# Kernel tuning notes

Hardware: AMD Instinct MI355X
Metric: run time of the kernel (lower is better)

The kernel has to match this reference:

```python
import jax, jax.numpy as jnp
import numpy as np

B, S, UNI, H, FLD = 64, 512, 1024, 1024, 256


def setup_inputs() -> dict:
    key = jax.random.key(0)
    ks = jax.random.split(key, 8)
    input_embeddings = jax.random.normal(ks[0], (B, S, UNI), dtype=jnp.float32)
    field_embeddings = jax.random.normal(ks[1], (B, S, FLD), dtype=jnp.float32)
    input_length = jax.random.randint(ks[2], (B,), 1, S + 1).astype(jnp.int32)
    # Force max length == S so the torch while-loop would run exactly S steps.
    input_length = input_length.at[0].set(S)
    std = 0.02
    W = jax.random.normal(ks[3], (UNI + H, 4 * H), dtype=jnp.float32) * std   # input+hidden -> i,j,f,o
    bW = jnp.zeros((4 * H,), dtype=jnp.float32)
    W1 = jax.random.normal(ks[4], (FLD, 2 * H), dtype=jnp.float32) * std      # field -> r,d
    bW1 = jnp.zeros((2 * H,), dtype=jnp.float32)
    return {
        "input_embeddings": input_embeddings,
        "field_embeddings": field_embeddings,
        "input_length": input_length,
        "W": W, "bW": bW, "W1": W1, "bW1": bW1,
    }


def reference(input_embeddings, field_embeddings, input_length, W, bW, W1, bW1):
    Bb, T, _ = input_embeddings.shape
    Hh = bW.shape[0] // 4
    # Field gate contribution is state-independent: precompute for all timesteps.
    fg = jnp.einsum('btf,fo->bto', field_embeddings, W1) + bW1      # [B,T,2H]
    r, d = jnp.split(fg, 2, axis=-1)
    field_term = jax.nn.sigmoid(r) * jnp.tanh(d)                    # [B,T,H]

    xs = jnp.swapaxes(input_embeddings, 0, 1)                       # [T,B,UNI]
    fts = jnp.swapaxes(field_term, 0, 1)                            # [T,B,H]
    # active[t,b] = t < input_length[b]  (mirrors `finished = t >= input_length`)
    active = jnp.arange(T, dtype=input_length.dtype)[:, None] < input_length[None, :]  # [T,B]

    h0 = jnp.zeros((Bb, Hh), dtype=input_embeddings.dtype)
    c0 = jnp.zeros((Bb, Hh), dtype=input_embeddings.dtype)

    def step(carry, inp):
        h, c = carry
        x_t, ft_t, act_t = inp
        gates = jnp.concatenate([x_t, h], axis=-1) @ W + bW         # [B,4H]
        i, j, f, o = jnp.split(gates, 4, axis=-1)
        c_new = jax.nn.sigmoid(f + 1.0) * c + jax.nn.sigmoid(i) * jnp.tanh(j) + ft_t
        h_new = jax.nn.sigmoid(o) * jnp.tanh(c_new)
        m = act_t[:, None]
        out = jnp.where(m, h_new, 0.0)                              # finished rows emit zeros
        h = jnp.where(m, h_new, h)                                  # finished rows keep prev state
        c = jnp.where(m, c_new, c)
        return (h, c), out

    (h_fin, c_fin), outs = jax.lax.scan(step, (h0, c0), (xs, fts, active))
    emit = jnp.swapaxes(outs, 0, 1)                                 # [B,T,H]
    return emit, (h_fin, c_fin)
```

## Files before the change

### kernel.cpp

```cpp
#include <hip/hip_runtime.h>

typedef unsigned short u16;
typedef __attribute__((ext_vector_type(8))) __bf16 bf16x8;
typedef __attribute__((ext_vector_type(4))) float f32x4;
typedef __attribute__((ext_vector_type(4))) unsigned int u32x4;
typedef __attribute__((ext_vector_type(2))) unsigned int u32x2;

#define GX_OFF   0ull
#define FT_OFF   268435456ull
#define WT_OFF   335544320ull
#define W1T_OFF  352321536ull
#define CB_OFF   352321536ull
#define HF_OFF   352583680ull
#define HB_OFF   353370112ull
#define WS_NEED  (HB_OFF + 262144ull)

#define NBLK 256

__device__ __forceinline__ float b2f(u16 u) {
    unsigned x = ((unsigned)u) << 16;
    return __builtin_bit_cast(float, x);
}
__device__ __forceinline__ u16 f2b(float f) {
    unsigned u = __builtin_bit_cast(unsigned, f);
    unsigned r = (u + 0x7FFFu + ((u >> 16) & 1u)) >> 16;
    return (u16)r;
}
__device__ __forceinline__ float fsigm(float x) {
    return __builtin_amdgcn_rcpf(1.f + __expf(-x));
}
__device__ __forceinline__ float ftanh2(float x) {
    return 2.f * __builtin_amdgcn_rcpf(1.f + __expf(-2.f * x)) - 1.f;
}
__device__ __forceinline__ bf16x8 ld_frag(const u16* p) {
    u32x4 v = *(const u32x4*)p;
    return __builtin_bit_cast(bf16x8, v);
}
__device__ __forceinline__ f32x4 mfma16(bf16x8 a, bf16x8 b, f32x4 c) {
    return __builtin_amdgcn_mfma_f32_16x16x32_bf16(a, b, c, 0, 0, 0);
}
__device__ __forceinline__ u32x4 cvt8(const float* p) {
    f32x4 a = *(const f32x4*)p;
    f32x4 b = *(const f32x4*)(p + 4);
    u32x4 r;
    r.x = (unsigned)f2b(a[0]) | ((unsigned)f2b(a[1]) << 16);
    r.y = (unsigned)f2b(a[2]) | ((unsigned)f2b(a[3]) << 16);
    r.z = (unsigned)f2b(b[0]) | ((unsigned)f2b(b[1]) << 16);
    r.w = (unsigned)f2b(b[2]) | ((unsigned)f2b(b[3]) << 16);
    return r;
}

__device__ __forceinline__ u32x4 ld16_coh(const u16* p) {
    u32x4 v;
    asm volatile("global_load_dwordx4 %0, %1, off sc0 sc1" : "=v"(v) : "v"(p));
    return v;
}
__device__ __forceinline__ void st2_coh(u16* p, u16 val) {
    unsigned v = val;
    asm volatile("global_store_short %0, %1, off sc0 sc1" :: "v"(p), "v"(v) : "memory");
}
__device__ __forceinline__ void st4_coh(unsigned* p, unsigned v) {
    asm volatile("global_store_dword %0, %1, off sc0 sc1" :: "v"(p), "v"(v) : "memory");
}
__device__ __forceinline__ unsigned ld4_coh_wait(const unsigned* p) {
    unsigned v;
    asm volatile("global_load_dword %0, %1, off sc0 sc1\n\ts_waitcnt vmcnt(0)"
                 : "=v"(v) : "v"(p) : "memory");
    return v;
}

__global__ void k_transpose(const float* __restrict__ in, u16* __restrict__ out, int R, int C) {
    __shared__ u16 tl[64][65];
    int tx = threadIdx.x, ty = threadIdx.y;
    int c0 = blockIdx.x * 64, r0 = blockIdx.y * 64;
#pragma unroll
    for (int i = 0; i < 16; i++) {
        int a = ty + i * 4;
        tl[a][tx] = f2b(in[(size_t)(r0 + a) * C + c0 + tx]);
    }
    __syncthreads();
#pragma unroll
    for (int i = 0; i < 16; i++) {
        int a = ty + i * 4;
        out[(size_t)(c0 + a) * R + r0 + tx] = tl[tx][a];
    }
}

__global__ __launch_bounds__(256) void k_field(const float* __restrict__ F, const u16* __restrict__ W1t,
                                               const float* __restrict__ bW1, const int* __restrict__ len,
                                               u16* __restrict__ ftw) {
    int m0 = blockIdx.y * 128;
    if ((m0 & 511) >= len[m0 >> 9]) return;
    int n0 = blockIdx.x * 64;
    __shared__ u16 As[128 * 40];
    __shared__ u16 Bs[128 * 40];
    int tid = threadIdx.x, w = tid >> 6, lane = tid & 63, quad = lane >> 4, l16 = lane & 15;
    f32x4 acc[2][8];
#pragma unroll
    for (int mt = 0; mt < 2; mt++)
#pragma unroll
        for (int nt = 0; nt < 8; nt++) acc[mt][nt] = (f32x4){0.f, 0.f, 0.f, 0.f};

    for (int kc = 0; kc < 8; kc++) {
        __syncthreads();
#pragma unroll
        for (int it = 0; it < 2; it++) {
            int q = tid + it * 256, row = q >> 2, sub = q & 3;
            u32x4 va = cvt8(F + (size_t)(m0 + row) * 256 + kc * 32 + sub * 8);
            *(u32x4*)(As + row * 40 + sub * 8) = va;
            int brow = (row < 64) ? (n0 + row) : (1024 + n0 + row - 64);
            u32x4 vb = *(const u32x4*)(W1t + (size_t)brow * 256 + kc * 32 + sub * 8);
            *(u32x4*)(Bs + row * 40 + sub * 8) = vb;
        }
        __syncthreads();
        bf16x8 af[2], bfr[8];
#pragma unroll
        for (int mt = 0; mt < 2; mt++) af[mt] = ld_frag(As + (w * 32 + mt * 16 + l16) * 40 + quad * 8);
#pragma unroll
        for (int nt = 0; nt < 8; nt++) bfr[nt] = ld_frag(Bs + (nt * 16 + l16) * 40 + quad * 8);
#pragma unroll
        for (int mt = 0; mt < 2; mt++)
#pragma unroll
            for (int nt = 0; nt < 8; nt++) acc[mt][nt] = mfma16(af[mt], bfr[nt], acc[mt][nt]);
    }
#pragma unroll
    for (int nth = 0; nth < 4; nth++) {
        float br = bW1[n0 + nth * 16 + l16];
        float bd = bW1[1024 + n0 + nth * 16 + l16];
#pragma unroll
        for (int mt = 0; mt < 2; mt++) {
#pragma unroll
            for (int j = 0; j < 4; j++) {
                int r = m0 + w * 32 + mt * 16 + quad * 4 + j;
                float rv = acc[mt][nth][j] + br;
                float dv = acc[mt][nth + 4][j] + bd;
                ftw[(size_t)r * 1024 + n0 + nth * 16 + l16] = f2b(fsigm(rv) * ftanh2(dv));
            }
        }
    }
}

__global__ __launch_bounds__(256) void k_xgemm(const float* __restrict__ X, const u16* __restrict__ Wt,
                                               const float* __restrict__ bWv, const int* __restrict__ len,
                                               u16* __restrict__ gx) {
    int m0 = blockIdx.y * 128;
    if ((m0 & 511) >= len[m0 >> 9]) return;
    int n0 = blockIdx.x * 128;
    __shared__ u16 As[128 * 40];
    __shared__ u16 Bs[128 * 40];
    int tid = threadIdx.x, w = tid >> 6, lane = tid & 63, quad = lane >> 4, l16 = lane & 15;
    int mq = (w & 1) * 64, nq = (w >> 1) * 64;
    f32x4 acc[4][4];
#pragma unroll
    for (int mt = 0; mt < 4; mt++)
#pragma unroll
        for (int nt = 0; nt < 4; nt++) acc[mt][nt] = (f32x4){0.f, 0.f, 0.f, 0.f};

    for (int kc = 0; kc < 32; kc++) {
        __syncthreads();
#pragma unroll
        for (int it = 0; it < 2; it++) {
            int q = tid + it * 256, row = q >> 2, sub = q & 3;
            u32x4 va = cvt8(X + (size_t)(m0 + row) * 1024 + kc * 32 + sub * 8);
            *(u32x4*)(As + row * 40 + sub * 8) = va;
            u32x4 vb = *(const u32x4*)(Wt + (size_t)(n0 + row) * 2048 + kc * 32 + sub * 8);
            *(u32x4*)(Bs + row * 40 + sub * 8) = vb;
        }
        __syncthreads();
        bf16x8 af[4], bfr[4];
#pragma unroll
        for (int mt = 0; mt < 4; mt++) af[mt] = ld_frag(As + (mq + mt * 16 + l16) * 40 + quad * 8);
#pragma unroll
        for (int nt = 0; nt < 4; nt++) bfr[nt] = ld_frag(Bs + (nq + nt * 16 + l16) * 40 + quad * 8);
#pragma unroll
        for (int mt = 0; mt < 4; mt++)
#pragma unroll
            for (int nt = 0; nt < 4; nt++) acc[mt][nt] = mfma16(af[mt], bfr[nt], acc[mt][nt]);
    }
#pragma unroll
    for (int nt = 0; nt < 4; nt++) {
        int gcol = n0 + nq + nt * 16 + l16;
        int hcol = gcol & 1023, g = gcol >> 10;
        float bw = bWv[gcol];
#pragma unroll
        for (int mt = 0; mt < 4; mt++) {
#pragma unroll
            for (int j = 0; j < 4; j++) {
                int r = m0 + mq + mt * 16 + quad * 4 + j;
                gx[(size_t)r * 4096 + hcol * 4 + g] = f2b(acc[mt][nt][j] + bw);
            }
        }
    }
}

__global__ void k_zero(u16* __restrict__ hbuf, float* __restrict__ cbuf, float* __restrict__ hfin) {
    int idx = blockIdx.x * 1024 + threadIdx.x;
    hbuf[idx] = 0; hbuf[65536 + idx] = 0;
    cbuf[idx] = 0.f; hfin[idx] = 0.f;
}

__global__ __launch_bounds__(256, 1) void k_lstm(const u16* __restrict__ Wt, const u16* __restrict__ gx,
                                                 const u16* __restrict__ ftw, const int* __restrict__ len,
                                                 float* __restrict__ out, u16* __restrict__ hbuf,
                                                 unsigned* __restrict__ bar) {
    __shared__ __align__(16) float red[4 * 64 * 20];
    int tid = threadIdx.x;
    int w = tid >> 6, lane = tid & 63, quad = lane >> 4, l16 = lane & 15;
    int blk = blockIdx.x;
    int bbg = blk & 3, wg = blk >> 2;

    bf16x8 breg[8][4];
#pragma unroll
    for (int kk = 0; kk < 8; kk++)
#pragma unroll
        for (int nt = 0; nt < 4; nt++) {
            size_t gcol = (size_t)nt * 1024 + wg * 16 + l16;
            breg[kk][nt] = ld_frag(Wt + gcol * 2048 + 1024 + w * 256 + kk * 32 + quad * 8);
        }

    int bbl = tid >> 4, hc = tid & 15;
    int bb = bbg * 16 + bbl;
    int Hcol = wg * 16 + hc;
    int mylen = len[bb];
    float hreg = 0.f, creg = 0.f;

    unsigned* myflag = bar + (((size_t)bbg << 6) | (size_t)wg) * 32;
    const unsigned* pollw = bar + (((size_t)bbg << 6) | (size_t)(w * 16 + (lane & 15))) * 32;

    u32x2 gq = *(const u32x2*)(gx + ((size_t)bb * 512) * 4096 + (size_t)Hcol * 4);
    float ftv = b2f(ftw[((size_t)bb * 512) * 1024 + Hcol]);

    for (int t = 0; t < 512; t++) {
        const u16* hb = hbuf + (t & 1) * 65536;
        u16* hbn = hbuf + ((t + 1) & 1) * 65536;

        u32x4 av[8];
#pragma unroll
        for (int kk = 0; kk < 8; kk++) {
            const u16* ap = hb + (size_t)(bbg * 16 + l16) * 1024 + w * 256 + kk * 32 + quad * 8;
            av[kk] = ld16_coh(ap);
        }
        asm volatile("s_waitcnt vmcnt(0)" ::: "memory");
        __builtin_amdgcn_sched_barrier(0);

        f32x4 acc[4];
#pragma unroll
        for (int nt = 0; nt < 4; nt++) acc[nt] = (f32x4){0.f, 0.f, 0.f, 0.f};
#pragma unroll
        for (int kk = 0; kk < 8; kk++) {
            bf16x8 af = __builtin_bit_cast(bf16x8, av[kk]);
#pragma unroll
            for (int nt = 0; nt < 4; nt++) acc[nt] = mfma16(af, breg[kk][nt], acc[nt]);
        }
#pragma unroll
        for (int nt = 0; nt < 4; nt++)
            *(f32x4*)&red[(w * 64 + nt * 16 + l16) * 20 + quad * 4] = acc[nt];
        __syncthreads();

        float G[4];
#pragma unroll
        for (int g = 0; g < 4; g++) {
            int c = g * 16 + hc;
            G[g] = red[(0 * 64 + c) * 20 + bbl] + red[(1 * 64 + c) * 20 + bbl]
                 + red[(2 * 64 + c) * 20 + bbl] + red[(3 * 64 + c) * 20 + bbl];
        }
        float iv = G[0] + b2f((u16)(gq.x & 0xffff));
        float jv = G[1] + b2f((u16)(gq.x >> 16));
        float fv = G[2] + b2f((u16)(gq.y & 0xffff));
        float ov = G[3] + b2f((u16)(gq.y >> 16));
        float cn = fsigm(fv + 1.f) * creg + fsigm(iv) * ftanh2(jv) + ftv;
        float hn = fsigm(ov) * ftanh2(cn);
        bool act = t < mylen;
        out[(size_t)bb * 524288 + (size_t)t * 1024 + Hcol] = act ? hn : 0.f;
        hreg = act ? hn : hreg;
        creg = act ? cn : creg;
        st2_coh(hbn + bb * 1024 + Hcol, f2b(hreg));

        if (t != 511) {
            asm volatile("s_waitcnt vmcnt(0)" ::: "memory");
            __syncthreads();
            unsigned gen = (unsigned)(t + 1);
            if (tid == 0) st4_coh(myflag, gen);
            size_t rowi = (size_t)bb * 512 + (t + 1);
            gq = *(const u32x2*)(gx + rowi * 4096 + (size_t)Hcol * 4);
            ftv = b2f(ftw[rowi * 1024 + Hcol]);
            for (;;) {
                unsigned v = ld4_coh_wait(pollw);
                if (__all((int)(v >= gen))) break;
                __builtin_amdgcn_s_sleep(1);
            }
        }
    }
    out[33554432 + (size_t)bb * 1024 + Hcol] = hreg;
    out[33554432 + 65536 + (size_t)bb * 1024 + Hcol] = creg;
}

__global__ __launch_bounds__(256) void k_step(const u16* __restrict__ Wt, const u16* __restrict__ gx,
                                              const u16* __restrict__ ftw, const int* __restrict__ len,
                                              float* __restrict__ out, u16* __restrict__ hbuf,
                                              float* __restrict__ cbuf, float* __restrict__ hfin, int t) {
    int wg = blockIdx.x;
    int tid = threadIdx.x, w = tid >> 6, lane = tid & 63, quad = lane >> 4, l16 = lane & 15;
    __shared__ float red[4 * 64 * 68];

    const u16* hb = hbuf + (t & 1) * 65536;
    u16* hbn = hbuf + ((t + 1) & 1) * 65536;

    f32x4 acc[4][4];
#pragma unroll
    for (int mt = 0; mt < 4; mt++)
#pragma unroll
        for (int nt = 0; nt < 4; nt++) acc[mt][nt] = (f32x4){0.f, 0.f, 0.f, 0.f};

#pragma unroll
    for (int kk = 0; kk < 8; kk++) {
        bf16x8 af[4], bq[4];
#pragma unroll
        for (int mt = 0; mt < 4; mt++)
            af[mt] = ld_frag(hb + (mt * 16 + l16) * 1024 + w * 256 + kk * 32 + quad * 8);
#pragma unroll
        for (int nt = 0; nt < 4; nt++) {
            int c = nt * 16 + l16;
            int gcol = (c & 3) * 1024 + wg * 16 + (c >> 2);
            bq[nt] = ld_frag(Wt + (size_t)gcol * 2048 + 1024 + w * 256 + kk * 32 + quad * 8);
        }
#pragma unroll
        for (int mt = 0; mt < 4; mt++)
#pragma unroll
            for (int nt = 0; nt < 4; nt++) acc[mt][nt] = mfma16(af[mt], bq[nt], acc[mt][nt]);
    }

#pragma unroll
    for (int mt = 0; mt < 4; mt++)
#pragma unroll
        for (int nt = 0; nt < 4; nt++)
            *(f32x4*)&red[(w * 64 + nt * 16 + l16) * 68 + mt * 16 + quad * 4] = acc[mt][nt];
    __syncthreads();

    int hc = tid & 15, rg = tid >> 4;
    int Hcol = wg * 16 + hc;
    f32x4 Gv[4];
#pragma unroll
    for (int g = 0; g < 4; g++) {
        int c = hc * 4 + g;
        f32x4 s = *(f32x4*)&red[(0 * 64 + c) * 68 + rg * 4];
#pragma unroll
        for (int wq = 1; wq < 4; wq++) s += *(f32x4*)&red[(wq * 64 + c) * 68 + rg * 4];
        Gv[g] = s;
    }

#pragma unroll
    for (int j = 0; j < 4; j++) {
        int bb = rg * 4 + j;
        size_t rowi = (size_t)bb * 512 + t;
        u32x2 gq = *(const u32x2*)(gx + rowi * 4096 + (size_t)Hcol * 4);
        float iv = Gv[0][j] + b2f((u16)(gq.x & 0xffff));
        float jv = Gv[1][j] + b2f((u16)(gq.x >> 16));
        float fv = Gv[2][j] + b2f((u16)(gq.y & 0xffff));
        float ov = Gv[3][j] + b2f((u16)(gq.y >> 16));
        float ftv = b2f(ftw[rowi * 1024 + Hcol]);
        float cprev = cbuf[bb * 1024 + Hcol];
        float hprev = hfin[bb * 1024 + Hcol];
        float cn = fsigm(fv + 1.f) * cprev + fsigm(iv) * ftanh2(jv) + ftv;
        float hn = fsigm(ov) * ftanh2(cn);
        bool act = t < len[bb];
        out[(size_t)bb * 524288 + (size_t)t * 1024 + Hcol] = act ? hn : 0.f;
        hbn[bb * 1024 + Hcol] = f2b(act ? hn : hprev);
        cbuf[bb * 1024 + Hcol] = act ? cn : cprev;
        hfin[bb * 1024 + Hcol] = act ? hn : hprev;
    }
}

__global__ void k_fin(const float* __restrict__ hfin, const float* __restrict__ cbuf,
                      float* __restrict__ out) {
    int idx = blockIdx.x * 1024 + threadIdx.x;
    out[33554432 + idx] = hfin[idx];
    out[33554432 + 65536 + idx] = cbuf[idx];
}

extern "C" void kernel_launch(void* const* d_in, const int* in_sizes, int n_in,
                              void* d_out, int out_size, void* d_ws, size_t ws_size,
                              hipStream_t stream) {
    (void)in_sizes; (void)n_in; (void)out_size;
    if (ws_size < WS_NEED) return;

    const float* X   = (const float*)d_in[0];
    const float* F   = (const float*)d_in[1];
    const int*   len = (const int*)d_in[2];
    const float* W   = (const float*)d_in[3];
    const float* bW  = (const float*)d_in[4];
    const float* W1  = (const float*)d_in[5];
    const float* bW1 = (const float*)d_in[6];
    float* out = (float*)d_out;

    char* ws = (char*)d_ws;
    u16*   gx   = (u16*)(ws + GX_OFF);
    u16*   ftw  = (u16*)(ws + FT_OFF);
    u16*   Wt   = (u16*)(ws + WT_OFF);
    u16*   W1t  = (u16*)(ws + W1T_OFF);
    float* cbuf = (float*)(ws + CB_OFF);
    float* hfin = (float*)(ws + HF_OFF);
    u16*   hbuf = (u16*)(ws + HB_OFF);

    k_transpose<<<dim3(64, 32), dim3(64, 4), 0, stream>>>(W, Wt, 2048, 4096);
    k_transpose<<<dim3(32, 4), dim3(64, 4), 0, stream>>>(W1, W1t, 256, 2048);
    k_field<<<dim3(16, 256), 256, 0, stream>>>(F, W1t, bW1, len, ftw);
    k_xgemm<<<dim3(32, 256), 256, 0, stream>>>(X, Wt, bW, len, gx);
    k_zero<<<64, 1024, 0, stream>>>(hbuf, cbuf, hfin);

    unsigned* bar = (unsigned*)cbuf;
    void* args[7] = {(void*)&Wt, (void*)&gx, (void*)&ftw, (void*)&len,
                     (void*)&out, (void*)&hbuf, (void*)&bar};
    hipError_t e = hipLaunchCooperativeKernel((const void*)k_lstm, dim3(NBLK), dim3(256),
                                              args, 0, stream);
    if (e != hipSuccess) {
        for (int t = 0; t < 512; t++)
            k_step<<<64, 256, 0, stream>>>(Wt, gx, ftw, len, out, hbuf, cbuf, hfin, t);
        k_fin<<<64, 1024, 0, stream>>>(hfin, cbuf, out);
    }
}
```

Before: 2.611 ms.

## Replace flag barrier with generation-tagged hidden state polling in persistent LSTM

Each hidden-state element is now stored as a 32-bit word that packs the step number in the high half and the bf16 value in the low half. Consumers spin directly on the hidden-state loads until every tag reaches the current step. This removes the per-step store drain, the extra workgroup barrier, the flag store and the separate flag poll. The LDS reduction buffer is double-buffered so one workgroup barrier per step is enough. In exchange, the hidden-state reads per step double in size, and the whole buffer is re-polled when any word is stale.

```diff
diff --git a/kernel.cpp b/kernel.cpp
--- a/kernel.cpp
+++ b/kernel.cpp
@@ -50,23 +50,13 @@
     return r;
 }
 
-__device__ __forceinline__ u32x4 ld16_coh(const u16* p) {
+__device__ __forceinline__ u32x4 ld16u_coh(const unsigned* p) {
     u32x4 v;
     asm volatile("global_load_dwordx4 %0, %1, off sc0 sc1" : "=v"(v) : "v"(p));
     return v;
 }
-__device__ __forceinline__ void st2_coh(u16* p, u16 val) {
-    unsigned v = val;
-    asm volatile("global_store_short %0, %1, off sc0 sc1" :: "v"(p), "v"(v) : "memory");
-}
 __device__ __forceinline__ void st4_coh(unsigned* p, unsigned v) {
     asm volatile("global_store_dword %0, %1, off sc0 sc1" :: "v"(p), "v"(v) : "memory");
-}
-__device__ __forceinline__ unsigned ld4_coh_wait(const unsigned* p) {
-    unsigned v;
-    asm volatile("global_load_dword %0, %1, off sc0 sc1\n\ts_waitcnt vmcnt(0)"
-                 : "=v"(v) : "v"(p) : "memory");
-    return v;
 }
 
 __global__ void k_transpose(const float* __restrict__ in, u16* __restrict__ out, int R, int C) {
@@ -201,9 +191,8 @@
 
 __global__ __launch_bounds__(256, 1) void k_lstm(const u16* __restrict__ Wt, const u16* __restrict__ gx,
                                                  const u16* __restrict__ ftw, const int* __restrict__ len,
-                                                 float* __restrict__ out, u16* __restrict__ hbuf,
-                                                 unsigned* __restrict__ bar) {
-    __shared__ __align__(16) float red[4 * 64 * 20];
+                                                 float* __restrict__ out, unsigned* __restrict__ hb32) {
+    __shared__ __align__(16) float red[2][4 * 64 * 20];
     int tid = threadIdx.x;
     int w = tid >> 6, lane = tid & 63, quad = lane >> 4, l16 = lane & 15;
     int blk = blockIdx.x;
@@ -224,45 +213,67 @@
     int mylen = len[bb];
     float hreg = 0.f, creg = 0.f;
 
-    unsigned* myflag = bar + (((size_t)bbg << 6) | (size_t)wg) * 32;
-    const unsigned* pollw = bar + (((size_t)bbg << 6) | (size_t)(w * 16 + (lane & 15))) * 32;
+    const unsigned* ab0 = hb32 + (size_t)(bbg * 16 + l16) * 1024 + w * 256 + quad * 8;
+    unsigned* hst0 = hb32 + (size_t)bb * 1024 + Hcol;
 
     u32x2 gq = *(const u32x2*)(gx + ((size_t)bb * 512) * 4096 + (size_t)Hcol * 4);
     float ftv = b2f(ftw[((size_t)bb * 512) * 1024 + Hcol]);
 
     for (int t = 0; t < 512; t++) {
-        const u16* hb = hbuf + (t & 1) * 65536;
-        u16* hbn = hbuf + ((t + 1) & 1) * 65536;
-
-        u32x4 av[8];
+        const unsigned* ab = ab0 + (size_t)(t & 1) * 65536;
+        unsigned gen = (unsigned)t;
+
+        u32x4 av[16];
+        for (;;) {
+#pragma unroll
+            for (int kk = 0; kk < 8; kk++) {
+                av[2 * kk]     = ld16u_coh(ab + kk * 32);
+                av[2 * kk + 1] = ld16u_coh(ab + kk * 32 + 4);
+            }
+            asm volatile("s_waitcnt vmcnt(0)" ::: "memory");
+            unsigned mn = 0xFFFFFFFFu;
+#pragma unroll
+            for (int j = 0; j < 16; j++) {
+                unsigned a = av[j].x < av[j].y ? av[j].x : av[j].y;
+                unsigned b = av[j].z < av[j].w ? av[j].z : av[j].w;
+                a = a < b ? a : b;
+                mn = mn < a ? mn : a;
+            }
+            if (__all((int)((mn >> 16) >= gen))) break;
+            __builtin_amdgcn_s_sleep(1);
+        }
+        __builtin_amdgcn_sched_barrier(0);
+
+        f32x4 acc[4];
+#pragma unroll
+        for (int nt = 0; nt < 4; nt++) acc[nt] = (f32x4){0.f, 0.f, 0.f, 0.f};
 #pragma unroll
         for (int kk = 0; kk < 8; kk++) {
-            const u16* ap = hb + (size_t)(bbg * 16 + l16) * 1024 + w * 256 + kk * 32 + quad * 8;
-            av[kk] = ld16_coh(ap);
-        }
-        asm volatile("s_waitcnt vmcnt(0)" ::: "memory");
+            u32x4 a = av[2 * kk], b = av[2 * kk + 1];
+            u32x4 fr;
+            fr.x = (a.x & 0xffffu) | (a.y << 16);
+            fr.y = (a.z & 0xffffu) | (a.w << 16);
+            fr.z = (b.x & 0xffffu) | (b.y << 16);
+            fr.w = (b.z & 0xffffu) | (b.w << 16);
+            bf16x8 af = __builtin_bit_cast(bf16x8, fr);
+#pragma unroll
+            for (int nt = 0; nt < 4; nt++) acc[nt] = mfma16(af, breg[kk][nt], acc[nt]);
+        }
+        float* rp = red[t & 1];
+#pragma unroll
+        for (int nt = 0; nt < 4; nt++)
+            *(f32x4*)&rp[(w * 64 + nt * 16 + l16) * 20 + quad * 4] = acc[nt];
+        asm volatile("s_waitcnt lgkmcnt(0)" ::: "memory");
         __builtin_amdgcn_sched_barrier(0);
-
-        f32x4 acc[4];
-#pragma unroll
-        for (int nt = 0; nt < 4; nt++) acc[nt] = (f32x4){0.f, 0.f, 0.f, 0.f};
-#pragma unroll
-        for (int kk = 0; kk < 8; kk++) {
-            bf16x8 af = __builtin_bit_cast(bf16x8, av[kk]);
-#pragma unroll
-            for (int nt = 0; nt < 4; nt++) acc[nt] = mfma16(af, breg[kk][nt], acc[nt]);
-        }
-#pragma unroll
-        for (int nt = 0; nt < 4; nt++)
-            *(f32x4*)&red[(w * 64 + nt * 16 + l16) * 20 + quad * 4] = acc[nt];
-        __syncthreads();
+        __builtin_amdgcn_s_barrier();
+        __builtin_amdgcn_sched_barrier(0);
 
         float G[4];
 #pragma unroll
         for (int g = 0; g < 4; g++) {
             int c = g * 16 + hc;
-            G[g] = red[(0 * 64 + c) * 20 + bbl] + red[(1 * 64 + c) * 20 + bbl]
-                 + red[(2 * 64 + c) * 20 + bbl] + red[(3 * 64 + c) * 20 + bbl];
+            G[g] = rp[(0 * 64 + c) * 20 + bbl] + rp[(1 * 64 + c) * 20 + bbl]
+                 + rp[(2 * 64 + c) * 20 + bbl] + rp[(3 * 64 + c) * 20 + bbl];
         }
         float iv = G[0] + b2f((u16)(gq.x & 0xffff));
         float jv = G[1] + b2f((u16)(gq.x >> 16));
@@ -271,24 +282,15 @@
         float cn = fsigm(fv + 1.f) * creg + fsigm(iv) * ftanh2(jv) + ftv;
         float hn = fsigm(ov) * ftanh2(cn);
         bool act = t < mylen;
-        out[(size_t)bb * 524288 + (size_t)t * 1024 + Hcol] = act ? hn : 0.f;
         hreg = act ? hn : hreg;
         creg = act ? cn : creg;
-        st2_coh(hbn + bb * 1024 + Hcol, f2b(hreg));
-
+        st4_coh(hst0 + (size_t)((t + 1) & 1) * 65536,
+                ((unsigned)(t + 1) << 16) | (unsigned)f2b(hreg));
+        out[(size_t)bb * 524288 + (size_t)t * 1024 + Hcol] = act ? hn : 0.f;
         if (t != 511) {
-            asm volatile("s_waitcnt vmcnt(0)" ::: "memory");
-            __syncthreads();
-            unsigned gen = (unsigned)(t + 1);
-            if (tid == 0) st4_coh(myflag, gen);
             size_t rowi = (size_t)bb * 512 + (t + 1);
             gq = *(const u32x2*)(gx + rowi * 4096 + (size_t)Hcol * 4);
             ftv = b2f(ftw[rowi * 1024 + Hcol]);
-            for (;;) {
-                unsigned v = ld4_coh_wait(pollw);
-                if (__all((int)(v >= gen))) break;
-                __builtin_amdgcn_s_sleep(1);
-            }
         }
     }
     out[33554432 + (size_t)bb * 1024 + Hcol] = hreg;
@@ -401,6 +403,7 @@
     float* cbuf = (float*)(ws + CB_OFF);
     float* hfin = (float*)(ws + HF_OFF);
     u16*   hbuf = (u16*)(ws + HB_OFF);
+    unsigned* hb32 = (unsigned*)(ws + CB_OFF);
 
     k_transpose<<<dim3(64, 32), dim3(64, 4), 0, stream>>>(W, Wt, 2048, 4096);
     k_transpose<<<dim3(32, 4), dim3(64, 4), 0, stream>>>(W1, W1t, 256, 2048);
@@ -408,9 +411,8 @@
     k_xgemm<<<dim3(32, 256), 256, 0, stream>>>(X, Wt, bW, len, gx);
     k_zero<<<64, 1024, 0, stream>>>(hbuf, cbuf, hfin);
 
-    unsigned* bar = (unsigned*)cbuf;
-    void* args[7] = {(void*)&Wt, (void*)&gx, (void*)&ftw, (void*)&len,
-                     (void*)&out, (void*)&hbuf, (void*)&bar};
+    void* args[6] = {(void*)&Wt, (void*)&gx, (void*)&ftw, (void*)&len,
+                     (void*)&out, (void*)&hb32};
     hipError_t e = hipLaunchCooperativeKernel((const void*)k_lstm, dim3(NBLK), dim3(256),
                                               args, 0, stream);
     if (e != hipSuccess) {
```

After: 2.871 ms. 1.1x slower.
